# Kernel tuning notes

Measured on AMD Instinct MI355X. Metric: run time of the kernel, lower is better.

The kernel has to match this reference:

```python
import jax, jax.numpy as jnp
import numpy as np

B, H, E_DIM, V = 512, 2048, 1024, 50257


def setup_inputs() -> dict:
    key = jax.random.key(0)
    ks = jax.random.split(key, 10)
    s_e = 1.0 / np.sqrt(E_DIM)
    s_h = 1.0 / np.sqrt(H)
    return {
        "inp": jax.random.randint(ks[0], (B,), 0, V),
        "h_0": jax.random.normal(ks[1], (B, H), jnp.float32) * 0.1,
        "c_0": jax.random.normal(ks[2], (B, H), jnp.float32) * 0.1,
        "E": jax.random.normal(ks[3], (V, E_DIM), jnp.float32),
        "Wx": jax.random.normal(ks[4], (4, H, E_DIM), jnp.float32) * s_e,
        "bx": jax.random.normal(ks[5], (4, H), jnp.float32) * s_e,
        "Wh": jax.random.normal(ks[6], (4, H, H), jnp.float32) * s_h,
        "bh": jax.random.normal(ks[7], (4, H), jnp.float32) * s_h,
        "Wd": jax.random.normal(ks[8], (V, H), jnp.float32) * s_h,
        "bd": jax.random.normal(ks[9], (V,), jnp.float32) * s_h,
    }


def reference(inp, h_0, c_0, E, Wx, bx, Wh, bh, Wd, bd):
    # Embedding lookup: [B, E_DIM]
    x = E[inp]
    # Two fused GEMMs for all 4 gates (gate order: f, i, o, c): [B, 4, H]
    gates = (jnp.einsum('be,ghe->bgh', x, Wx) + bx[None]
             + jnp.einsum('bh,gkh->bgk', h_0, Wh) + bh[None])
    f_g = jax.nn.sigmoid(gates[:, 0])
    i_g = jax.nn.sigmoid(gates[:, 1])
    o_g = jax.nn.sigmoid(gates[:, 2])
    c_tilda = jnp.tanh(gates[:, 3])
    cx = f_g * c_0 + i_g * c_tilda
    hx = o_g * jnp.tanh(cx)
    out = hx @ Wd.T + bd  # [B, V]
    return out, hx, cx
```

## Files before the change

kernel.cpp:

```cpp
#include <hip/hip_runtime.h>
#include <hip/hip_bf16.h>

using bf16x8 = __attribute__((ext_vector_type(8))) short;
using f32x4  = __attribute__((ext_vector_type(4))) float;

#define DEVI __device__ __forceinline__

DEVI unsigned short bf16r(float f)
{
    return __builtin_bit_cast(unsigned short, __float2bfloat16(f));
}

DEVI bf16x8 cvt8(const f32x4 a, const f32x4 b)
{
    bf16x8 r;
#pragma unroll
    for (int j = 0; j < 4; ++j) {
        r[j]     = (short)bf16r(a[j]);
        r[4 + j] = (short)bf16r(b[j]);
    }
    return r;
}

__global__ __launch_bounds__(256) void k_gather(const float* __restrict__ E,
                                                const int* __restrict__ inp,
                                                unsigned short* __restrict__ x)
{
    const int b = blockIdx.x;
    const long r = inp[b];
    const f32x4 v = ((const f32x4*)(E + r * 1024L))[threadIdx.x];
    ushort4 o;
    o.x = bf16r(v[0]); o.y = bf16r(v[1]); o.z = bf16r(v[2]); o.w = bf16r(v[3]);
    ((ushort4*)(x + (long)b * 1024L))[threadIdx.x] = o;
}

__global__ __launch_bounds__(256) void k_cvt(const float* __restrict__ in,
                                             unsigned short* __restrict__ out)
{
    const long i = (blockIdx.x * 256L + threadIdx.x) * 8;
    const f32x4 a = *(const f32x4*)(in + i);
    const f32x4 b = *(const f32x4*)(in + i + 4);
    *(bf16x8*)(out + i) = cvt8(a, b);
}


DEVI void mfma_tile(const char* sA, const char* sB, int l, int wr, int wc,
                    f32x4 (&acc)[4][4])
{
#pragma unroll
    for (int ks = 0; ks < 2; ++ks) {
        bf16x8 af[4], bq[4];
#pragma unroll
        for (int m = 0; m < 4; ++m) {
            const int ar = wr * 64 + m * 16 + (l & 15);
            const int j  = ks * 4 + (l >> 4);
            af[m] = *(const bf16x8*)(sA + ar * 128 + ((j ^ (ar & 7)) << 4));
        }
#pragma unroll
        for (int n = 0; n < 4; ++n) {
            const int br = wc * 64 + n * 16 + (l & 15);
            const int rx = ((br & 7) << 1) | ((br >> 3) & 1);
            const int f  = ks * 4 + (l >> 4);
            const f32x4 lo = *(const f32x4*)(sB + br * 256 + (((2 * f)     ^ rx) << 4));
            const f32x4 hi = *(const f32x4*)(sB + br * 256 + (((2 * f + 1) ^ rx) << 4));
            bq[n] = cvt8(lo, hi);
        }
#pragma unroll
        for (int m = 0; m < 4; ++m)
#pragma unroll
            for (int n = 0; n < 4; ++n)
                acc[m][n] = __builtin_amdgcn_mfma_f32_16x16x32_bf16(
                    af[m], bq[n], acc[m][n], 0, 0, 0);
    }
}

template <bool CLAMP>
DEVI void gemm_core(const unsigned short* __restrict__ A, long lda, long arow0,
                    const float* __restrict__ B, long ldb, long brow0, long bmax,
                    int ntiles, long kbase, int t, char* sA, char* sB,
                    f32x4 (&acc)[4][4])
{
    const int l = t & 63;
    const int wr = (t >> 7) & 1, wc = (t >> 6) & 1;

    const unsigned short* ap[4];
    const float* bp[8];
#pragma unroll
    for (int i = 0; i < 4; ++i) {
        const int g = i * 256 + t, row = g >> 3, js = g & 7;
        ap[i] = A + (arow0 + row) * lda + kbase + (long)((js ^ (row & 7)) * 8);
    }
#pragma unroll
    for (int i = 0; i < 8; ++i) {
        const int g = i * 256 + t, row = g >> 4, sx = g & 15;
        const int rx = ((row & 7) << 1) | ((row >> 3) & 1);
        long br = brow0 + row;
        if (CLAMP) br = (br < bmax) ? br : (bmax - 1);
        bp[i] = B + br * ldb + kbase + (long)((sx ^ rx) * 4);
    }

    for (int ti = 0; ti < ntiles; ++ti) {
        __syncthreads();
#pragma unroll
        for (int i = 0; i < 4; ++i)
            __builtin_amdgcn_global_load_lds(
                (const __attribute__((address_space(1))) void*)(ap[i]),
                (__attribute__((address_space(3))) void*)(sA + (i * 256 + t) * 16),
                16, 0, 0);
#pragma unroll
        for (int i = 0; i < 8; ++i)
            __builtin_amdgcn_global_load_lds(
                (const __attribute__((address_space(1))) void*)(bp[i]),
                (__attribute__((address_space(3))) void*)(sB + (i * 256 + t) * 16),
                16, 0, 0);
        __syncthreads();
#pragma unroll
        for (int i = 0; i < 4; ++i) ap[i] += 64;
#pragma unroll
        for (int i = 0; i < 8; ++i) bp[i] += 64;
        mfma_tile(sA, sB, l, wr, wc, acc);
    }
}

__global__ __launch_bounds__(256, 3) void k_gates(
    const unsigned short* __restrict__ xb, const float* __restrict__ Wx,
    const unsigned short* __restrict__ h0b, const float* __restrict__ Wh,
    float* __restrict__ g0, float* __restrict__ g1, float* __restrict__ g2)
{
    __shared__ __align__(16) char sA[128 * 128];
    __shared__ __align__(16) char sB[128 * 256];
    const int t = threadIdx.x;
    const int bid = blockIdx.x;
    const int xcd = bid & 7, slot = bid >> 3;
    const int L = xcd * 96 + slot;
    const int mtile = L & 3;
    const int rest = L >> 2;
    const int ntile = rest & 63;
    const int z = rest >> 6;

    const unsigned short* A; const float* B; long lda, ldb, kbase; float* C;
    if (z == 0)      { A = xb;  lda = 1024; B = Wx; ldb = 1024; kbase = 0;    C = g0; }
    else if (z == 1) { A = h0b; lda = 2048; B = Wh; ldb = 2048; kbase = 0;    C = g1; }
    else             { A = h0b; lda = 2048; B = Wh; ldb = 2048; kbase = 1024; C = g2; }

    f32x4 acc[4][4] = {};
    gemm_core<false>(A, lda, (long)mtile * 128, B, ldb, (long)ntile * 128,
                     1L << 40, 16, kbase, t, sA, sB, acc);

    const int l = t & 63;
    const int wr = (t >> 7) & 1, wc = (t >> 6) & 1;
    const int lc = l & 15, r4 = (l >> 4) * 4;
#pragma unroll
    for (int n = 0; n < 4; ++n) {
        const long col = (long)ntile * 128 + wc * 64 + n * 16 + lc;
#pragma unroll
        for (int m = 0; m < 4; ++m) {
            const long row = (long)mtile * 128 + wr * 64 + m * 16 + r4;
#pragma unroll
            for (int r = 0; r < 4; ++r)
                C[(row + r) * 8192 + col] = acc[m][n][r];
        }
    }
}

__global__ __launch_bounds__(256, 3) void k_dec(
    const unsigned short* __restrict__ hxb, const float* __restrict__ Wd,
    const float* __restrict__ bd, float* __restrict__ out)
{
    __shared__ __align__(16) char sA[128 * 128];
    __shared__ __align__(16) char sB[128 * 256];
    const int t = threadIdx.x;
    const int bid = blockIdx.x;
    const int xcd = bid & 7, slot = bid >> 3;
    const int L = xcd * 196 + (xcd < 4 ? xcd : 4) + slot;
    const int mtile = L & 3;
    const int ntile = L >> 2;
    const long N = 50257;

    f32x4 acc[4][4] = {};
    gemm_core<true>(hxb, 2048, (long)mtile * 128, Wd, 2048, (long)ntile * 128,
                    N, 32, 0, t, sA, sB, acc);

    const int l = t & 63;
    const int wr = (t >> 7) & 1, wc = (t >> 6) & 1;
    const int lc = l & 15, r4 = (l >> 4) * 4;
#pragma unroll
    for (int n = 0; n < 4; ++n) {
        const long col = (long)ntile * 128 + wc * 64 + n * 16 + lc;
        if (col >= N) continue;
        const float bias = bd[col];
#pragma unroll
        for (int m = 0; m < 4; ++m) {
            const long row = (long)mtile * 128 + wr * 64 + m * 16 + r4;
#pragma unroll
            for (int r = 0; r < 4; ++r)
                out[(row + r) * N + col] = acc[m][n][r] + bias;
        }
    }
}

__global__ __launch_bounds__(256) void k_lstm(
    const float* __restrict__ g0, const float* __restrict__ g1,
    const float* __restrict__ g2, const float* __restrict__ bx,
    const float* __restrict__ bh, const float* __restrict__ c0,
    float* __restrict__ hx, float* __restrict__ cx,
    unsigned short* __restrict__ hxb)
{
    const int i = blockIdx.x * 256 + threadIdx.x;
    const int b = i >> 9;
    const int hc = (i & 511) << 2;
    const long base = (long)b * 8192;

    f32x4 g[4];
#pragma unroll
    for (int gi = 0; gi < 4; ++gi) {
        const long off = base + gi * 2048 + hc;
        const int boff = gi * 2048 + hc;
        g[gi] = *(const f32x4*)(g0 + off);
        g[gi] += *(const f32x4*)(g1 + off);
        g[gi] += *(const f32x4*)(g2 + off);
        g[gi] += *(const f32x4*)(bx + boff);
        g[gi] += *(const f32x4*)(bh + boff);
    }
    const f32x4 c0v = *(const f32x4*)(c0 + (long)b * 2048 + hc);

    f32x4 cv, hv;
    ushort4 hb;
#pragma unroll
    for (int j = 0; j < 4; ++j) {
        const float fg = 1.f / (1.f + __expf(-g[0][j]));
        const float ig = 1.f / (1.f + __expf(-g[1][j]));
        const float og = 1.f / (1.f + __expf(-g[2][j]));
        const float e2 = __expf(2.f * g[3][j]);
        const float ct = 1.f - 2.f / (e2 + 1.f);
        const float c  = fg * c0v[j] + ig * ct;
        const float e2c = __expf(2.f * c);
        const float th  = 1.f - 2.f / (e2c + 1.f);
        cv[j] = c;
        hv[j] = og * th;
    }
    hb.x = bf16r(hv[0]); hb.y = bf16r(hv[1]); hb.z = bf16r(hv[2]); hb.w = bf16r(hv[3]);

    const long o = (long)b * 2048 + hc;
    *(f32x4*)(cx + o) = cv;
    *(f32x4*)(hx + o) = hv;
    *(ushort4*)(hxb + o) = hb;
}

extern "C" void kernel_launch(void* const* d_in, const int* in_sizes, int n_in,
                              void* d_out, int out_size, void* d_ws, size_t ws_size,
                              hipStream_t stream)
{
    const int*   inp = (const int*)d_in[0];
    const float* h0  = (const float*)d_in[1];
    const float* c0  = (const float*)d_in[2];
    const float* E   = (const float*)d_in[3];
    const float* Wx  = (const float*)d_in[4];
    const float* bx  = (const float*)d_in[5];
    const float* Wh  = (const float*)d_in[6];
    const float* bh  = (const float*)d_in[7];
    const float* Wd  = (const float*)d_in[8];
    const float* bd  = (const float*)d_in[9];

    float* out = (float*)d_out;
    float* hx  = out + 512L * 50257L;
    float* cx  = hx + 512L * 2048L;

    unsigned short* xb  = (unsigned short*)out;
    float* g0 = out + (1L << 20);
    float* g1 = out + (5L << 20);
    float* g2 = out + (9L << 20);
    unsigned short* h0b = (unsigned short*)(out + (13L << 20));
    unsigned short* hxb = (unsigned short*)d_ws;

    k_gather<<<512, 256, 0, stream>>>(E, inp, xb);
    k_cvt<<<512, 256, 0, stream>>>(h0, h0b);

    k_gates<<<768, 256, 0, stream>>>(xb, Wx, h0b, Wh, g0, g1, g2);

    k_lstm<<<1024, 256, 0, stream>>>(g0, g1, g2, bx, bh, c0, hx, cx, hxb);

    k_dec<<<1572, 256, 0, stream>>>(hxb, Wd, bd, out);
}
```

Before: 282.8 us.

## Convert B tiles to bf16 in registers before LDS, prefetching next tile

```diff
diff --git a/kernel.cpp b/kernel.cpp
--- a/kernel.cpp
+++ b/kernel.cpp
@@ -44,6 +44,11 @@
 }
 
 
+DEVI bf16x8 lds_frag(const char* lds, int row, int j)
+{
+    return *(const bf16x8*)(lds + row * 128 + ((j ^ (row & 7)) << 4));
+}
+
 DEVI void mfma_tile(const char* sA, const char* sB, int l, int wr, int wc,
                     f32x4 (&acc)[4][4])
 {
@@ -51,20 +56,11 @@
     for (int ks = 0; ks < 2; ++ks) {
         bf16x8 af[4], bq[4];
 #pragma unroll
-        for (int m = 0; m < 4; ++m) {
-            const int ar = wr * 64 + m * 16 + (l & 15);
-            const int j  = ks * 4 + (l >> 4);
-            af[m] = *(const bf16x8*)(sA + ar * 128 + ((j ^ (ar & 7)) << 4));
-        }
-#pragma unroll
-        for (int n = 0; n < 4; ++n) {
-            const int br = wc * 64 + n * 16 + (l & 15);
-            const int rx = ((br & 7) << 1) | ((br >> 3) & 1);
-            const int f  = ks * 4 + (l >> 4);
-            const f32x4 lo = *(const f32x4*)(sB + br * 256 + (((2 * f)     ^ rx) << 4));
-            const f32x4 hi = *(const f32x4*)(sB + br * 256 + (((2 * f + 1) ^ rx) << 4));
-            bq[n] = cvt8(lo, hi);
-        }
+        for (int m = 0; m < 4; ++m)
+            af[m] = lds_frag(sA, wr * 64 + m * 16 + (l & 15), ks * 4 + (l >> 4));
+#pragma unroll
+        for (int n = 0; n < 4; ++n)
+            bq[n] = lds_frag(sB, wc * 64 + n * 16 + (l & 15), ks * 4 + (l >> 4));
 #pragma unroll
         for (int m = 0; m < 4; ++m)
 #pragma unroll
@@ -84,19 +80,26 @@
     const int wr = (t >> 7) & 1, wc = (t >> 6) & 1;
 
     const unsigned short* ap[4];
-    const float* bp[8];
 #pragma unroll
     for (int i = 0; i < 4; ++i) {
         const int g = i * 256 + t, row = g >> 3, js = g & 7;
         ap[i] = A + (arow0 + row) * lda + kbase + (long)((js ^ (row & 7)) * 8);
     }
-#pragma unroll
-    for (int i = 0; i < 8; ++i) {
-        const int g = i * 256 + t, row = g >> 4, sx = g & 15;
-        const int rx = ((row & 7) << 1) | ((row >> 3) & 1);
+    const float* bp[4];
+#pragma unroll
+    for (int i = 0; i < 4; ++i) {
+        const int g = i * 256 + t, row = g >> 3, j = g & 7;
         long br = brow0 + row;
         if (CLAMP) br = (br < bmax) ? br : (bmax - 1);
-        bp[i] = B + br * ldb + kbase + (long)((sx ^ rx) * 4);
+        bp[i] = B + br * ldb + kbase + (long)(j * 8);
+    }
+
+    f32x4 br0[4], br1[4];
+#pragma unroll
+    for (int i = 0; i < 4; ++i) {
+        br0[i] = *(const f32x4*)bp[i];
+        br1[i] = *(const f32x4*)(bp[i] + 4);
+        bp[i] += 64;
     }
 
     for (int ti = 0; ti < ntiles; ++ti) {
@@ -108,16 +111,21 @@
                 (__attribute__((address_space(3))) void*)(sA + (i * 256 + t) * 16),
                 16, 0, 0);
 #pragma unroll
-        for (int i = 0; i < 8; ++i)
-            __builtin_amdgcn_global_load_lds(
-                (const __attribute__((address_space(1))) void*)(bp[i]),
-                (__attribute__((address_space(3))) void*)(sB + (i * 256 + t) * 16),
-                16, 0, 0);
+        for (int i = 0; i < 4; ++i) {
+            const int g = i * 256 + t, row = g >> 3, j = g & 7;
+            *(bf16x8*)(sB + row * 128 + ((j ^ (row & 7)) << 4)) = cvt8(br0[i], br1[i]);
+        }
         __syncthreads();
 #pragma unroll
         for (int i = 0; i < 4; ++i) ap[i] += 64;
-#pragma unroll
-        for (int i = 0; i < 8; ++i) bp[i] += 64;
+        if (ti + 1 < ntiles) {
+#pragma unroll
+            for (int i = 0; i < 4; ++i) {
+                br0[i] = *(const f32x4*)bp[i];
+                br1[i] = *(const f32x4*)(bp[i] + 4);
+                bp[i] += 64;
+            }
+        }
         mfma_tile(sA, sB, l, wr, wc, acc);
     }
 }
@@ -128,7 +136,7 @@
     float* __restrict__ g0, float* __restrict__ g1, float* __restrict__ g2)
 {
     __shared__ __align__(16) char sA[128 * 128];
-    __shared__ __align__(16) char sB[128 * 256];
+    __shared__ __align__(16) char sB[128 * 128];
     const int t = threadIdx.x;
     const int bid = blockIdx.x;
     const int xcd = bid & 7, slot = bid >> 3;
@@ -168,7 +176,7 @@
     const float* __restrict__ bd, float* __restrict__ out)
 {
     __shared__ __align__(16) char sA[128 * 128];
-    __shared__ __align__(16) char sB[128 * 256];
+    __shared__ __align__(16) char sB[128 * 128];
     const int t = threadIdx.x;
     const int bid = blockIdx.x;
     const int xcd = bid & 7, slot = bid >> 3;
```

After: 296.1 us. 4.7% more time.

## Switch GEMM tiles to 256x128 with K-step 32 to halve weight re-reads

Applied to the files above, without the earlier changes.

```diff
diff --git a/kernel.cpp b/kernel.cpp
--- a/kernel.cpp
+++ b/kernel.cpp
@@ -34,8 +34,8 @@
     ((ushort4*)(x + (long)b * 1024L))[threadIdx.x] = o;
 }
 
-__global__ __launch_bounds__(256) void k_cvt(const float* __restrict__ in,
-                                             unsigned short* __restrict__ out)
+__global__ __launch_bounds__(256) void k_cvtn(const float* __restrict__ in,
+                                              unsigned short* __restrict__ out)
 {
     const long i = (blockIdx.x * 256L + threadIdx.x) * 8;
     const f32x4 a = *(const f32x4*)(in + i);
@@ -44,81 +44,76 @@
 }
 
 
-DEVI void mfma_tile(const char* sA, const char* sB, int l, int wr, int wc,
-                    f32x4 (&acc)[4][4])
-{
-#pragma unroll
-    for (int ks = 0; ks < 2; ++ks) {
-        bf16x8 af[4], bq[4];
-#pragma unroll
-        for (int m = 0; m < 4; ++m) {
-            const int ar = wr * 64 + m * 16 + (l & 15);
-            const int j  = ks * 4 + (l >> 4);
-            af[m] = *(const bf16x8*)(sA + ar * 128 + ((j ^ (ar & 7)) << 4));
-        }
-#pragma unroll
-        for (int n = 0; n < 4; ++n) {
-            const int br = wc * 64 + n * 16 + (l & 15);
-            const int rx = ((br & 7) << 1) | ((br >> 3) & 1);
-            const int f  = ks * 4 + (l >> 4);
-            const f32x4 lo = *(const f32x4*)(sB + br * 256 + (((2 * f)     ^ rx) << 4));
-            const f32x4 hi = *(const f32x4*)(sB + br * 256 + (((2 * f + 1) ^ rx) << 4));
-            bq[n] = cvt8(lo, hi);
-        }
-#pragma unroll
-        for (int m = 0; m < 4; ++m)
-#pragma unroll
-            for (int n = 0; n < 4; ++n)
-                acc[m][n] = __builtin_amdgcn_mfma_f32_16x16x32_bf16(
-                    af[m], bq[n], acc[m][n], 0, 0, 0);
-    }
+DEVI void mfma_tile256(const char* sA, const char* sB, int l, int wr, int wc,
+                       f32x4 (&acc)[8][4])
+{
+    const int j = l >> 4;
+    bf16x8 af[8], bq[4];
+#pragma unroll
+    for (int m = 0; m < 8; ++m) {
+        const int ar = wr * 128 + m * 16 + (l & 15);
+        af[m] = *(const bf16x8*)(sA + ar * 64 + ((j ^ ((ar >> 1) & 3)) << 4));
+    }
+#pragma unroll
+    for (int n = 0; n < 4; ++n) {
+        const int br = wc * 64 + n * 16 + (l & 15);
+        const int rx = br & 7;
+        const f32x4 lo = *(const f32x4*)(sB + br * 128 + (((2 * j)     ^ rx) << 4));
+        const f32x4 hi = *(const f32x4*)(sB + br * 128 + (((2 * j + 1) ^ rx) << 4));
+        bq[n] = cvt8(lo, hi);
+    }
+#pragma unroll
+    for (int m = 0; m < 8; ++m)
+#pragma unroll
+        for (int n = 0; n < 4; ++n)
+            acc[m][n] = __builtin_amdgcn_mfma_f32_16x16x32_bf16(
+                af[m], bq[n], acc[m][n], 0, 0, 0);
 }
 
 template <bool CLAMP>
-DEVI void gemm_core(const unsigned short* __restrict__ A, long lda, long arow0,
-                    const float* __restrict__ B, long ldb, long brow0, long bmax,
-                    int ntiles, long kbase, int t, char* sA, char* sB,
-                    f32x4 (&acc)[4][4])
+DEVI void gemm_core256(const unsigned short* __restrict__ A, long lda, long arow0,
+                       const float* __restrict__ B, long ldb, long brow0,
+                       long bmax, int nt, long kbase, int t,
+                       char* sA, char* sB, f32x4 (&acc)[8][4])
 {
     const int l = t & 63;
     const int wr = (t >> 7) & 1, wc = (t >> 6) & 1;
 
     const unsigned short* ap[4];
-    const float* bp[8];
 #pragma unroll
     for (int i = 0; i < 4; ++i) {
-        const int g = i * 256 + t, row = g >> 3, js = g & 7;
-        ap[i] = A + (arow0 + row) * lda + kbase + (long)((js ^ (row & 7)) * 8);
-    }
-#pragma unroll
-    for (int i = 0; i < 8; ++i) {
-        const int g = i * 256 + t, row = g >> 4, sx = g & 15;
-        const int rx = ((row & 7) << 1) | ((row >> 3) & 1);
+        const int g = i * 256 + t, row = g >> 2, j = g & 3;
+        ap[i] = A + (arow0 + row) * lda + kbase + (long)((j ^ ((row >> 1) & 3)) * 8);
+    }
+    const float* bp[4];
+#pragma unroll
+    for (int i = 0; i < 4; ++i) {
+        const int g = i * 256 + t, row = g >> 3, s = g & 7;
         long br = brow0 + row;
         if (CLAMP) br = (br < bmax) ? br : (bmax - 1);
-        bp[i] = B + br * ldb + kbase + (long)((sx ^ rx) * 4);
-    }
-
-    for (int ti = 0; ti < ntiles; ++ti) {
+        bp[i] = B + br * ldb + kbase + (long)((s ^ (row & 7)) * 4);
+    }
+
+    for (int ti = 0; ti < nt; ++ti) {
         __syncthreads();
 #pragma unroll
-        for (int i = 0; i < 4; ++i)
+        for (int i = 0; i < 4; ++i) {
             __builtin_amdgcn_global_load_lds(
                 (const __attribute__((address_space(1))) void*)(ap[i]),
                 (__attribute__((address_space(3))) void*)(sA + (i * 256 + t) * 16),
                 16, 0, 0);
-#pragma unroll
-        for (int i = 0; i < 8; ++i)
+            ap[i] += 32;
+        }
+#pragma unroll
+        for (int i = 0; i < 4; ++i) {
             __builtin_amdgcn_global_load_lds(
                 (const __attribute__((address_space(1))) void*)(bp[i]),
                 (__attribute__((address_space(3))) void*)(sB + (i * 256 + t) * 16),
                 16, 0, 0);
+            bp[i] += 32;
+        }
         __syncthreads();
-#pragma unroll
-        for (int i = 0; i < 4; ++i) ap[i] += 64;
-#pragma unroll
-        for (int i = 0; i < 8; ++i) bp[i] += 64;
-        mfma_tile(sA, sB, l, wr, wc, acc);
+        mfma_tile256(sA, sB, l, wr, wc, acc);
     }
 }
 
@@ -127,25 +122,25 @@
     const unsigned short* __restrict__ h0b, const float* __restrict__ Wh,
     float* __restrict__ g0, float* __restrict__ g1, float* __restrict__ g2)
 {
-    __shared__ __align__(16) char sA[128 * 128];
-    __shared__ __align__(16) char sB[128 * 256];
+    __shared__ __align__(16) char sA[16384];
+    __shared__ __align__(16) char sB[16384];
     const int t = threadIdx.x;
     const int bid = blockIdx.x;
     const int xcd = bid & 7, slot = bid >> 3;
-    const int L = xcd * 96 + slot;
-    const int mtile = L & 3;
-    const int rest = L >> 2;
-    const int ntile = rest & 63;
-    const int z = rest >> 6;
+    const int L = xcd * 48 + slot;
+    const int z = L >> 7;
+    const int rest = L & 127;
+    const int mtile = rest & 1;
+    const int ntile = rest >> 1;
 
     const unsigned short* A; const float* B; long lda, ldb, kbase; float* C;
     if (z == 0)      { A = xb;  lda = 1024; B = Wx; ldb = 1024; kbase = 0;    C = g0; }
     else if (z == 1) { A = h0b; lda = 2048; B = Wh; ldb = 2048; kbase = 0;    C = g1; }
     else             { A = h0b; lda = 2048; B = Wh; ldb = 2048; kbase = 1024; C = g2; }
 
-    f32x4 acc[4][4] = {};
-    gemm_core<false>(A, lda, (long)mtile * 128, B, ldb, (long)ntile * 128,
-                     1L << 40, 16, kbase, t, sA, sB, acc);
+    f32x4 acc[8][4] = {};
+    gemm_core256<false>(A, lda, (long)mtile * 256, B, ldb, (long)ntile * 128,
+                        1L << 40, 32, kbase, t, sA, sB, acc);
 
     const int l = t & 63;
     const int wr = (t >> 7) & 1, wc = (t >> 6) & 1;
@@ -154,8 +149,8 @@
     for (int n = 0; n < 4; ++n) {
         const long col = (long)ntile * 128 + wc * 64 + n * 16 + lc;
 #pragma unroll
-        for (int m = 0; m < 4; ++m) {
-            const long row = (long)mtile * 128 + wr * 64 + m * 16 + r4;
+        for (int m = 0; m < 8; ++m) {
+            const long row = (long)mtile * 256 + wr * 128 + m * 16 + r4;
 #pragma unroll
             for (int r = 0; r < 4; ++r)
                 C[(row + r) * 8192 + col] = acc[m][n][r];
@@ -167,19 +162,20 @@
     const unsigned short* __restrict__ hxb, const float* __restrict__ Wd,
     const float* __restrict__ bd, float* __restrict__ out)
 {
-    __shared__ __align__(16) char sA[128 * 128];
-    __shared__ __align__(16) char sB[128 * 256];
+    __shared__ __align__(16) char sA[16384];
+    __shared__ __align__(16) char sB[16384];
     const int t = threadIdx.x;
     const int bid = blockIdx.x;
     const int xcd = bid & 7, slot = bid >> 3;
-    const int L = xcd * 196 + (xcd < 4 ? xcd : 4) + slot;
-    const int mtile = L & 3;
-    const int ntile = L >> 2;
+    const int L = xcd * 100 + slot;
+    if (L >= 786) return;
+    const int mtile = L & 1;
+    const int ntile = L >> 1;
     const long N = 50257;
 
-    f32x4 acc[4][4] = {};
-    gemm_core<true>(hxb, 2048, (long)mtile * 128, Wd, 2048, (long)ntile * 128,
-                    N, 32, 0, t, sA, sB, acc);
+    f32x4 acc[8][4] = {};
+    gemm_core256<true>(hxb, 2048, (long)mtile * 256, Wd, 2048, (long)ntile * 128,
+                       N, 64, 0, t, sA, sB, acc);
 
     const int l = t & 63;
     const int wr = (t >> 7) & 1, wc = (t >> 6) & 1;
@@ -190,8 +186,8 @@
         if (col >= N) continue;
         const float bias = bd[col];
 #pragma unroll
-        for (int m = 0; m < 4; ++m) {
-            const long row = (long)mtile * 128 + wr * 64 + m * 16 + r4;
+        for (int m = 0; m < 8; ++m) {
+            const long row = (long)mtile * 256 + wr * 128 + m * 16 + r4;
 #pragma unroll
             for (int r = 0; r < 4; ++r)
                 out[(row + r) * N + col] = acc[m][n][r] + bias;
@@ -274,11 +270,11 @@
     unsigned short* hxb = (unsigned short*)d_ws;
 
     k_gather<<<512, 256, 0, stream>>>(E, inp, xb);
-    k_cvt<<<512, 256, 0, stream>>>(h0, h0b);
-
-    k_gates<<<768, 256, 0, stream>>>(xb, Wx, h0b, Wh, g0, g1, g2);
+    k_cvtn<<<512, 256, 0, stream>>>(h0, h0b);
+
+    k_gates<<<384, 256, 0, stream>>>(xb, Wx, h0b, Wh, g0, g1, g2);
 
     k_lstm<<<1024, 256, 0, stream>>>(g0, g1, g2, bx, bh, c0, hx, cx, hxb);
 
-    k_dec<<<1572, 256, 0, stream>>>(hxb, Wd, bd, out);
-}
+    k_dec<<<800, 256, 0, stream>>>(hxb, Wd, bd, out);
+}
```

Result: slower. 428.9 us (+51.7%).
